# Performance work log

Hardware: AMD Instinct MI355X
Metric: run time of the kernel (lower is better)

Reference implementation:

```python
import jax, jax.numpy as jnp
import numpy as np

D_MODEL, HEADS, D_FF = 768, 12, 3072
D_K = D_MODEL // HEADS
EPS = 1e-6


def _norm(x, alpha, bias):
    # NormalizationLayer: scalar alpha/bias, torch.std is unbiased (ddof=1)
    mean = jnp.mean(x, axis=-1, keepdims=True)
    std = jnp.std(x, axis=-1, ddof=1, keepdims=True)
    return alpha * (x - mean) / (std + EPS) + bias


def setup_inputs() -> dict:
    key = jax.random.key(0)
    ks = jax.random.split(key, 16)
    B, S = 2, 4096
    x = jax.random.normal(ks[0], (B, S, D_MODEL), dtype=jnp.float32)
    mask = jax.random.randint(ks[1], (B, 1, 1, S), 0, 2, dtype=jnp.int32)
    w = lambda k, o, i: (jax.random.normal(k, (o, i), dtype=jnp.float32) * 0.02)
    return {
        "x": x, "mask": mask,
        "wq": w(ks[2], D_MODEL, D_MODEL), "bq": jnp.zeros((D_MODEL,), jnp.float32),
        "wk": w(ks[3], D_MODEL, D_MODEL), "bk": jnp.zeros((D_MODEL,), jnp.float32),
        "wv": w(ks[4], D_MODEL, D_MODEL), "bv": jnp.zeros((D_MODEL,), jnp.float32),
        "wo": w(ks[5], D_MODEL, D_MODEL), "bo": jnp.zeros((D_MODEL,), jnp.float32),
        "w1": w(ks[6], D_FF, D_MODEL), "b1": jnp.zeros((D_FF,), jnp.float32),
        "w2": w(ks[7], D_MODEL, D_FF), "b2": jnp.zeros((D_MODEL,), jnp.float32),
        "alpha1": jnp.ones((1,), jnp.float32), "beta1": jnp.ones((1,), jnp.float32),
        "alpha2": jnp.ones((1,), jnp.float32), "beta2": jnp.ones((1,), jnp.float32),
    }


def reference(x, mask, wq, bq, wk, bk, wv, bv, wo, bo, w1, b1, w2, b2,
              alpha1, beta1, alpha2, beta2):
    B, S, _ = x.shape

    # --- residual connection 0: pre-norm + self-attention ---
    h = _norm(x, alpha1, beta1)
    q = (h @ wq.T + bq).reshape(B, S, HEADS, D_K).transpose(0, 2, 1, 3)  # [B,H,S,dk]
    k = (h @ wk.T + bk).reshape(B, S, HEADS, D_K).transpose(0, 2, 1, 3)
    v = (h @ wv.T + bv).reshape(B, S, HEADS, D_K).transpose(0, 2, 1, 3)
    scores = jnp.einsum('bhqd,bhkd->bhqk', q, k) / jnp.sqrt(jnp.float32(D_K))
    scores = jnp.where(mask == 0, jnp.float32(-1e9), scores)
    attn = jax.nn.softmax(scores, axis=-1)
    ctx = jnp.einsum('bhqk,bhkd->bhqd', attn, v)
    ctx = ctx.transpose(0, 2, 1, 3).reshape(B, S, D_MODEL)
    x = x + (ctx @ wo.T + bo)

    # --- residual connection 1: pre-norm + FFN ---
    h = _norm(x, alpha2, beta2)
    ff = jax.nn.relu(h @ w1.T + b1) @ w2.T + b2
    return x + ff
```

## Files before the change

kernel.cpp:

```cpp
#include <hip/hip_runtime.h>
#include <hip/hip_bf16.h>
#include <math.h>


typedef __hip_bfloat16 bf16;
typedef short short8 __attribute__((ext_vector_type(8)));
typedef short short4v __attribute__((ext_vector_type(4)));
typedef float f32x4 __attribute__((ext_vector_type(4)));

#define MFMA(A, B, C) __builtin_amdgcn_mfma_f32_16x16x32_bf16(A, B, C, 0, 0, 0)

__device__ __forceinline__ void gl_lds16(const void* g, void* l) {
  __builtin_amdgcn_global_load_lds(
      (__attribute__((address_space(1))) void*)g,
      (__attribute__((address_space(3))) void*)l, 16, 0, 0);
}

__device__ __forceinline__ short f2b(float f) {
  bf16 h = __float2bfloat16(f);
  return *reinterpret_cast<short*>(&h);
}

__global__ __launch_bounds__(256)
void prep_all(const float* __restrict__ wq, const float* __restrict__ wk,
              const float* __restrict__ wv, const float* __restrict__ wo,
              const float* __restrict__ w1, const float* __restrict__ w2,
              const float* __restrict__ bq, const float* __restrict__ bk,
              const float* __restrict__ bv, const int* __restrict__ mask,
              bf16* __restrict__ wqkvb, bf16* __restrict__ wob,
              bf16* __restrict__ w1b, bf16* __restrict__ w2b,
              float* __restrict__ bqkv,
              int* __restrict__ pos_g, int* __restrict__ nch_g,
              float* __restrict__ biasc,
              bf16* __restrict__ kc, bf16* __restrict__ vtc)
{
  const int t = threadIdx.x;
  if (blockIdx.x < 2) {
    const int b = blockIdx.x;
    const int* mb = mask + b * 4096;
    __shared__ int lsum[256];
    int loc = 0;
    int mv[16];
#pragma unroll
    for (int j = 0; j < 16; j++) { mv[j] = mb[t * 16 + j] ? 1 : 0; loc += mv[j]; }
    lsum[t] = loc;
    __syncthreads();
    for (int off = 1; off < 256; off <<= 1) {
      int v = (t >= off) ? lsum[t - off] : 0;
      __syncthreads();
      lsum[t] += v;
      __syncthreads();
    }
    const int nvalid = lsum[255];
    int base = lsum[t] - loc;
#pragma unroll
    for (int j = 0; j < 16; j++) {
      pos_g[b * 4096 + t * 16 + j] = mv[j] ? base : -1;
      if (mv[j]) base++;
    }
    const int npad = (nvalid + 63) & ~63;
    if (t == 0) nch_g[b] = npad >> 6;
    for (int i = t; i < 4096; i += 256)
      biasc[b * 4096 + i] = (i < nvalid) ? 0.f : -1e9f;
    const int npv = npad - nvalid;
    if (npv > 0) {
      const int krows = 12 * npv;
      const short8 z = {};
      for (int task = t; task < krows * 8; task += 256) {
        const int rr = task >> 3, cc = task & 7;
        const int hh = rr / npv, r = nvalid + rr % npv;
        *(short8*)&kc[(((long)(b * 12 + hh) * 4096) + r) * 64 + cc * 8] = z;
      }
      const int vrows = 12 * 64;
      for (int task = t; task < vrows * npv; task += 256) {
        const int row = task / npv, j = nvalid + task % npv;
        const int hh = row >> 6, d = row & 63;
        vtc[((long)((b * 12 + hh) * 64 + d)) * 4096 + j] = __float2bfloat16(0.f);
      }
    }
    return;
  }
  const int i = (blockIdx.x - 2) * 256 + t;
  const int W = 147456;
  const int F = 589824;
  const float* src; bf16* dst; int off;
  if (i < W)          { src = wq; dst = wqkvb;           off = i; }
  else if (i < 2*W)   { src = wk; dst = wqkvb + 589824;  off = i - W; }
  else if (i < 3*W)   { src = wv; dst = wqkvb + 1179648; off = i - 2*W; }
  else if (i < 4*W)   { src = wo; dst = wob;             off = i - 3*W; }
  else if (i < 4*W+F) { src = w1; dst = w1b;             off = i - 4*W; }
  else                { src = w2; dst = w2b;             off = i - 4*W - F; }
  float4 v = ((const float4*)src)[off];
  short4v o;
  o.x = f2b(v.x); o.y = f2b(v.y); o.z = f2b(v.z); o.w = f2b(v.w);
  ((short4v*)dst)[off] = o;
  if (i < 2304)
    bqkv[i] = (i < 768) ? bq[i] : (i < 1536 ? bk[i - 768] : bv[i - 1536]);
}

template<typename INT>
__global__ __launch_bounds__(256)
void ln_kernel(const INT* __restrict__ x, bf16* __restrict__ out,
               const float* __restrict__ alpha, const float* __restrict__ beta)
{
  const int row = blockIdx.x;
  const long base = (long)row * 768;
  const int t = threadIdx.x;
  float v[3]; float s = 0.f, ss = 0.f;
#pragma unroll
  for (int i = 0; i < 3; i++) {
    v[i] = (float)x[base + t + i * 256];
    s += v[i]; ss += v[i] * v[i];
  }
#pragma unroll
  for (int off = 32; off > 0; off >>= 1) {
    s  += __shfl_down(s, off);
    ss += __shfl_down(ss, off);
  }
  __shared__ float red[8];
  __shared__ float stats[2];
  const int w = t >> 6;
  if ((t & 63) == 0) { red[w] = s; red[4 + w] = ss; }
  __syncthreads();
  if (t == 0) {
    float S  = red[0] + red[1] + red[2] + red[3];
    float SS = red[4] + red[5] + red[6] + red[7];
    float mean = S * (1.f / 768.f);
    float var = fmaxf((SS - 768.f * mean * mean) * (1.f / 767.f), 0.f);
    stats[0] = mean;
    stats[1] = 1.f / (sqrtf(var) + 1e-6f);
  }
  __syncthreads();
  const float mean = stats[0], rinv = stats[1];
  const float a = alpha[0], b = beta[0];
#pragma unroll
  for (int i = 0; i < 3; i++)
    out[base + t + i * 256] = __float2bfloat16(a * (v[i] - mean) * rinv + b);
}

template<int MODE, int TM, typename RT, typename OUTT>
__global__ __launch_bounds__(256)
void gemm_bt(const bf16* __restrict__ A, const bf16* __restrict__ W,
             const float* __restrict__ bias, const RT* __restrict__ R,
             OUTT* __restrict__ Cout, int M, int N, int K)
{
  constexpr int MI = TM / 32;
  __shared__ __align__(16) bf16 sA[TM * 32];
  __shared__ __align__(16) bf16 sB[128 * 32];
  const int t = threadIdx.x;
  const int w = t >> 6, lane = t & 63;
  const int lr = lane & 15, quad = lane >> 4;
  const int tm = blockIdx.x * TM, tn = blockIdx.y * 128;
  const int wm = (w >> 1) * (MI * 16), wn = (w & 1) * 64;

  const int srow = w * 16 + (lane >> 2);
  const int scol = (lane & 3) * 8;
  const bf16* Ap = A + (long)(tm + srow) * K + scol;
  const bf16* Wp = W + (long)(tn + srow) * K + scol;
  bf16* sAp = &sA[srow * 32 + scol];
  bf16* sBp = &sB[srow * 32 + scol];
  const long half = (long)64 * K;

  f32x4 acc[MI][4] = {};

  for (int kb = 0; kb < K; kb += 32) {
    gl_lds16(Ap + kb, sAp);
    if (TM == 128) gl_lds16(Ap + kb + half, sAp + 64 * 32);
    gl_lds16(Wp + kb, sBp);
    gl_lds16(Wp + kb + half, sBp + 64 * 32);
    __syncthreads();
    short8 af[MI], bfr[4];
#pragma unroll
    for (int i = 0; i < MI; i++)
      af[i] = *(const short8*)&sA[(wm + i * 16 + lr) * 32 + quad * 8];
#pragma unroll
    for (int j = 0; j < 4; j++)
      bfr[j] = *(const short8*)&sB[(wn + j * 16 + lr) * 32 + quad * 8];
#pragma unroll
    for (int i = 0; i < MI; i++)
#pragma unroll
      for (int j = 0; j < 4; j++)
        acc[i][j] = MFMA(af[i], bfr[j], acc[i][j]);
    __syncthreads();
  }

#pragma unroll
  for (int i = 0; i < MI; i++) {
#pragma unroll
    for (int j = 0; j < 4; j++) {
      const int col = tn + wn + j * 16 + lr;
      const float bv = bias[col];
#pragma unroll
      for (int r = 0; r < 4; r++) {
        const int m = tm + wm + i * 16 + quad * 4 + r;
        float vv = acc[i][j][r] + bv;
        if (MODE == 1) vv = fmaxf(vv, 0.f);
        if (MODE == 4) vv += (float)R[(long)m * N + col];
        Cout[(long)m * N + col] = (OUTT)vv;
      }
    }
  }
}

__global__ __launch_bounds__(256)
void gemm_qkv(const bf16* __restrict__ A, const bf16* __restrict__ W,
              const float* __restrict__ bias, const int* __restrict__ pos_g,
              bf16* __restrict__ Qo, bf16* __restrict__ Kc, bf16* __restrict__ Vtc)
{
  const int K = 768;
  __shared__ __align__(16) bf16 sA[128 * 32];
  __shared__ __align__(16) bf16 sB[128 * 32];
  const int t = threadIdx.x;
  const int w = t >> 6, lane = t & 63;
  const int lr = lane & 15, quad = lane >> 4;
  const int tm = blockIdx.x * 128, tn = blockIdx.y * 128;
  const int wm = (w >> 1) * 64, wn = (w & 1) * 64;

  const int srow = w * 16 + (lane >> 2);
  const int scol = (lane & 3) * 8;
  const bf16* Ap = A + (long)(tm + srow) * K + scol;
  const bf16* Wp = W + (long)(tn + srow) * K + scol;
  bf16* sAp = &sA[srow * 32 + scol];
  bf16* sBp = &sB[srow * 32 + scol];
  const long half = (long)64 * K;

  f32x4 acc[4][4] = {};

  for (int kb = 0; kb < K; kb += 32) {
    gl_lds16(Ap + kb, sAp);
    gl_lds16(Ap + kb + half, sAp + 64 * 32);
    gl_lds16(Wp + kb, sBp);
    gl_lds16(Wp + kb + half, sBp + 64 * 32);
    __syncthreads();
    short8 af[4], bfr[4];
#pragma unroll
    for (int i = 0; i < 4; i++)
      af[i] = *(const short8*)&sA[(wm + i * 16 + lr) * 32 + quad * 8];
#pragma unroll
    for (int j = 0; j < 4; j++)
      bfr[j] = *(const short8*)&sB[(wn + j * 16 + lr) * 32 + quad * 8];
#pragma unroll
    for (int i = 0; i < 4; i++)
#pragma unroll
      for (int j = 0; j < 4; j++)
        acc[i][j] = MFMA(af[i], bfr[j], acc[i][j]);
    __syncthreads();
  }

  const int region = (tn >= 1536) ? 2 : (tn >= 768 ? 1 : 0);
#pragma unroll
  for (int i = 0; i < 4; i++) {
#pragma unroll
    for (int j = 0; j < 4; j++) {
      const int col = tn + wn + j * 16 + lr;
      const int c768 = col - region * 768;
      const int hh = c768 >> 6, d = c768 & 63;
      const float bv = bias[col];
#pragma unroll
      for (int r = 0; r < 4; r++) {
        const int m = tm + wm + i * 16 + quad * 4 + r;
        const int bb = m >> 12, sdx = m & 4095;
        float vv = acc[i][j][r] + bv;
        if (region == 0) {
          vv *= 0.125f;
          Qo[((long)(bb * 12 + hh) * 4096 + sdx) * 64 + d] = __float2bfloat16(vv);
        } else {
          const int p_ = pos_g[bb * 4096 + sdx];
          if (p_ >= 0) {
            if (region == 1)
              Kc[((long)(bb * 12 + hh) * 4096 + p_) * 64 + d] = __float2bfloat16(vv);
            else
              Vtc[((long)(bb * 12 + hh) * 64 + d) * 4096 + p_] = __float2bfloat16(vv);
          }
        }
      }
    }
  }
}

__global__ __launch_bounds__(256)
void attn_kernel(const bf16* __restrict__ Q, const bf16* __restrict__ Kg,
                 const bf16* __restrict__ Vt, const float* __restrict__ biasc,
                 const int* __restrict__ nch_g, bf16* __restrict__ ctx)
{
  __shared__ __align__(16) bf16 sK[64 * 72];
  __shared__ __align__(16) bf16 sV[64 * 72];
  __shared__ __align__(16) bf16 sP[4][32 * 72];

  const int t = threadIdx.x, w = t >> 6, lane = t & 63;
  const int lr = lane & 15, quad = lane >> 4;
  const int bh = blockIdx.y, b = bh / 12, hh = bh % 12;
  const int qb = blockIdx.x * 128 + w * 32;
  const long bh_s = (long)bh * 4096;
  const float* bg = biasc + b * 4096;
  const int nch = nch_g[b];

  short8 qf[2][2];
#pragma unroll
  for (int qt = 0; qt < 2; qt++) {
    const bf16* qp = Q + (bh_s + qb + qt * 16 + lr) * 64 + quad * 8;
    qf[qt][0] = *(const short8*)qp;
    qf[qt][1] = *(const short8*)(qp + 32);
  }

  float l_part[2][4] = {};
  f32x4 O[2][4] = {};

  const int srow = t >> 3;
  const int scol = (t & 7) * 8;
  const bf16* kp0 = Kg + (bh_s + srow) * 64 + scol;
  const bf16* kp1 = Kg + (bh_s + srow + 32) * 64 + scol;
  const bf16* vp0 = Vt + ((long)bh * 64 + srow) * 4096 + scol;
  const bf16* vp1 = Vt + ((long)bh * 64 + srow + 32) * 4096 + scol;

  for (int ci = 0; ci < nch; ci++) {
    const int kc = ci * 64;
    short8 k0 = *(const short8*)(kp0 + (long)kc * 64);
    short8 k1 = *(const short8*)(kp1 + (long)kc * 64);
    short8 v0 = *(const short8*)(vp0 + kc);
    short8 v1 = *(const short8*)(vp1 + kc);
    float bb[4];
#pragma unroll
    for (int kt = 0; kt < 4; kt++) bb[kt] = bg[kc + kt * 16 + lr];
    __syncthreads();
    *(short8*)&sK[srow * 72 + scol]        = k0;
    *(short8*)&sK[(srow + 32) * 72 + scol] = k1;
    *(short8*)&sV[srow * 72 + scol]        = v0;
    *(short8*)&sV[(srow + 32) * 72 + scol] = v1;
    __syncthreads();

    f32x4 s[2][4] = {};
#pragma unroll
    for (int kt = 0; kt < 4; kt++) {
      short8 kfa = *(const short8*)&sK[(kt * 16 + lr) * 72 + quad * 8];
      short8 kfb = *(const short8*)&sK[(kt * 16 + lr) * 72 + 32 + quad * 8];
      s[0][kt] = MFMA(qf[0][0], kfa, s[0][kt]);
      s[0][kt] = MFMA(qf[0][1], kfb, s[0][kt]);
      s[1][kt] = MFMA(qf[1][0], kfa, s[1][kt]);
      s[1][kt] = MFMA(qf[1][1], kfb, s[1][kt]);
    }

#pragma unroll
    for (int kt = 0; kt < 4; kt++) {
#pragma unroll
      for (int qt = 0; qt < 2; qt++) {
#pragma unroll
        for (int r = 0; r < 4; r++) {
          const float p = __expf(s[qt][kt][r] + bb[kt]);
          l_part[qt][r] += p;
          sP[w][(qt * 16 + quad * 4 + r) * 72 + kt * 16 + lr] = __float2bfloat16(p);
        }
      }
    }

    short8 pf[2][2];
#pragma unroll
    for (int qt = 0; qt < 2; qt++) {
      pf[qt][0] = *(const short8*)&sP[w][(qt * 16 + lr) * 72 + quad * 8];
      pf[qt][1] = *(const short8*)&sP[w][(qt * 16 + lr) * 72 + 32 + quad * 8];
    }
#pragma unroll
    for (int j = 0; j < 4; j++) {
      short8 vfa = *(const short8*)&sV[(j * 16 + lr) * 72 + quad * 8];
      short8 vfb = *(const short8*)&sV[(j * 16 + lr) * 72 + 32 + quad * 8];
      O[0][j] = MFMA(pf[0][0], vfa, O[0][j]);
      O[0][j] = MFMA(pf[0][1], vfb, O[0][j]);
      O[1][j] = MFMA(pf[1][0], vfa, O[1][j]);
      O[1][j] = MFMA(pf[1][1], vfb, O[1][j]);
    }
  }

#pragma unroll
  for (int qt = 0; qt < 2; qt++) {
#pragma unroll
    for (int r = 0; r < 4; r++) {
      float l = l_part[qt][r];
#pragma unroll
      for (int off = 1; off < 16; off <<= 1) l += __shfl_xor(l, off, 16);
      const float il = (l > 0.f) ? 1.f / l : 0.f;
      const int q = qb + qt * 16 + quad * 4 + r;
      bf16* cp = ctx + ((long)(b * 4096 + q)) * 768 + hh * 64 + lr;
#pragma unroll
      for (int j = 0; j < 4; j++)
        cp[j * 16] = __float2bfloat16(O[qt][j][r] * il);
    }
  }
}

extern "C" void kernel_launch(void* const* d_in, const int* in_sizes, int n_in,
                              void* d_out, int out_size, void* d_ws, size_t ws_size,
                              hipStream_t stream)
{
  (void)in_sizes; (void)n_in; (void)out_size; (void)ws_size;
  const float* x    = (const float*)d_in[0];
  const int*   mask = (const int*)  d_in[1];
  const float* wq = (const float*)d_in[2];  const float* bq = (const float*)d_in[3];
  const float* wk = (const float*)d_in[4];  const float* bk = (const float*)d_in[5];
  const float* wv = (const float*)d_in[6];  const float* bv = (const float*)d_in[7];
  const float* wo = (const float*)d_in[8];  const float* bo = (const float*)d_in[9];
  const float* w1 = (const float*)d_in[10]; const float* b1 = (const float*)d_in[11];
  const float* w2 = (const float*)d_in[12]; const float* b2 = (const float*)d_in[13];
  const float* alpha1 = (const float*)d_in[14]; const float* beta1 = (const float*)d_in[15];
  const float* alpha2 = (const float*)d_in[16]; const float* beta2 = (const float*)d_in[17];
  float* out = (float*)d_out;

  const long WSZ = (long)768 * 768 * 2;
  const long W1SZ = (long)3072 * 768 * 2;
  const long SZB = (long)8192 * 768 * 2;
  char* ws = (char*)d_ws;
  bf16* wqkvb = (bf16*)(ws);
  bf16* wob = (bf16*)(ws + 3 * WSZ);
  bf16* w1b = (bf16*)(ws + 4 * WSZ);
  bf16* w2b = (bf16*)(ws + 4 * WSZ + W1SZ);
  char* aux = ws + 4 * WSZ + 2 * W1SZ;
  float* bqkv   = (float*)(aux);
  int*   pos_g  = (int*)(aux + 16384);
  float* biasc  = (float*)(aux + 49152);
  int*   nch_g  = (int*)(aux + 81920);
  const long BASE = 16l << 20;
  bf16* h   = (bf16*)(ws + BASE);
  bf16* qws = (bf16*)(ws + BASE + 1 * SZB);
  bf16* kcw = (bf16*)(ws + BASE + 2 * SZB);
  bf16* vtc = (bf16*)(ws + BASE + 3 * SZB);
  bf16* ctx = (bf16*)(ws + BASE + 4 * SZB);
  bf16* x1  = (bf16*)(ws + BASE + 5 * SZB);
  bf16* ff  = qws;

  dim3 blk(256);

  hipLaunchKernelGGL(prep_all, dim3(6914), blk, 0, stream,
                     wq, wk, wv, wo, w1, w2, bq, bk, bv, mask,
                     wqkvb, wob, w1b, w2b, bqkv, pos_g, nch_g, biasc, kcw, vtc);

  hipLaunchKernelGGL((ln_kernel<float>), dim3(8192), blk, 0, stream, x, h, alpha1, beta1);
  hipLaunchKernelGGL(gemm_qkv, dim3(64, 18), blk, 0, stream, h, wqkvb, bqkv, pos_g, qws, kcw, vtc);
  hipLaunchKernelGGL(attn_kernel, dim3(32, 24), blk, 0, stream, qws, kcw, vtc, biasc, nch_g, ctx);
  hipLaunchKernelGGL((gemm_bt<4, 64, float, bf16>), dim3(128, 6), blk, 0, stream, ctx, wob, bo, x, x1, 8192, 768, 768);
  hipLaunchKernelGGL((ln_kernel<bf16>), dim3(8192), blk, 0, stream, x1, h, alpha2, beta2);
  hipLaunchKernelGGL((gemm_bt<1, 128, float, bf16>), dim3(64, 24), blk, 0, stream, h, w1b, b1, (const float*)nullptr, ff, 8192, 3072, 768);
  hipLaunchKernelGGL((gemm_bt<4, 64, bf16, float>), dim3(128, 6), blk, 0, stream, ff, w2b, b2, x1, out, 8192, 768, 3072);
}
```

Before: 425.9 us.

## Double-buffer attention K/V via async LDS loads with swizzled layout and exp2

```diff
diff --git a/kernel.cpp b/kernel.cpp
--- a/kernel.cpp
+++ b/kernel.cpp
@@ -9,6 +9,12 @@
 typedef float f32x4 __attribute__((ext_vector_type(4)));
 
 #define MFMA(A, B, C) __builtin_amdgcn_mfma_f32_16x16x32_bf16(A, B, C, 0, 0, 0)
+
+#if __has_builtin(__builtin_amdgcn_exp2f)
+#define EXP2(x) __builtin_amdgcn_exp2f(x)
+#else
+#define EXP2(x) exp2f(x)
+#endif
 
 __device__ __forceinline__ void gl_lds16(const void* g, void* l) {
   __builtin_amdgcn_global_load_lds(
@@ -262,7 +268,7 @@
         const int bb = m >> 12, sdx = m & 4095;
         float vv = acc[i][j][r] + bv;
         if (region == 0) {
-          vv *= 0.125f;
+          vv *= 0.18033688011112042f;
           Qo[((long)(bb * 12 + hh) * 4096 + sdx) * 64 + d] = __float2bfloat16(vv);
         } else {
           const int p_ = pos_g[bb * 4096 + sdx];
@@ -283,9 +289,9 @@
                  const bf16* __restrict__ Vt, const float* __restrict__ biasc,
                  const int* __restrict__ nch_g, bf16* __restrict__ ctx)
 {
-  __shared__ __align__(16) bf16 sK[64 * 72];
-  __shared__ __align__(16) bf16 sV[64 * 72];
-  __shared__ __align__(16) bf16 sP[4][32 * 72];
+  __shared__ __align__(16) bf16 sK[2][64 * 64];
+  __shared__ __align__(16) bf16 sV[2][64 * 64];
+  __shared__ __align__(16) bf16 sP[4][32 * 64];
 
   const int t = threadIdx.x, w = t >> 6, lane = t & 63;
   const int lr = lane & 15, quad = lane >> 4;
@@ -294,6 +300,7 @@
   const long bh_s = (long)bh * 4096;
   const float* bg = biasc + b * 4096;
   const int nch = nch_g[b];
+  bf16* sPw = sP[w];
 
   short8 qf[2][2];
 #pragma unroll
@@ -303,72 +310,94 @@
     qf[qt][1] = *(const short8*)(qp + 32);
   }
 
+  const int rA = w * 16 + (lane >> 3), rB = rA + 8;
+  const int c8 = lane & 7;
+  const int sigA = ((rA & 15) << 2) + (rA >> 4);
+  const int sigB = ((rB & 15) << 2) + (rB >> 4);
+  const bf16* kA = Kg + (bh_s + sigA) * 64 + ((c8 ^ (rA & 7)) << 3);
+  const bf16* kB = Kg + (bh_s + sigB) * 64 + ((c8 ^ (rB & 7)) << 3);
+  const bf16* vA = Vt + ((long)bh * 64 + rA) * 4096 + ((c8 ^ (rA & 7)) << 3);
+  const bf16* vB = Vt + ((long)bh * 64 + rB) * 4096 + ((c8 ^ (rB & 7)) << 3);
+  const int ldsA = (w * 16) * 64 + lane * 8;
+  const int ldsB = ldsA + 8 * 64;
+
+  const int cA = (quad * 8) ^ ((lr & 7) << 3);
+
   float l_part[2][4] = {};
   f32x4 O[2][4] = {};
 
-  const int srow = t >> 3;
-  const int scol = (t & 7) * 8;
-  const bf16* kp0 = Kg + (bh_s + srow) * 64 + scol;
-  const bf16* kp1 = Kg + (bh_s + srow + 32) * 64 + scol;
-  const bf16* vp0 = Vt + ((long)bh * 64 + srow) * 4096 + scol;
-  const bf16* vp1 = Vt + ((long)bh * 64 + srow + 32) * 4096 + scol;
-
-  for (int ci = 0; ci < nch; ci++) {
-    const int kc = ci * 64;
-    short8 k0 = *(const short8*)(kp0 + (long)kc * 64);
-    short8 k1 = *(const short8*)(kp1 + (long)kc * 64);
-    short8 v0 = *(const short8*)(vp0 + kc);
-    short8 v1 = *(const short8*)(vp1 + kc);
-    float bb[4];
-#pragma unroll
-    for (int kt = 0; kt < 4; kt++) bb[kt] = bg[kc + kt * 16 + lr];
-    __syncthreads();
-    *(short8*)&sK[srow * 72 + scol]        = k0;
-    *(short8*)&sK[(srow + 32) * 72 + scol] = k1;
-    *(short8*)&sV[srow * 72 + scol]        = v0;
-    *(short8*)&sV[(srow + 32) * 72 + scol] = v1;
-    __syncthreads();
-
+  auto stage = [&](int kc, int buf) {
+    gl_lds16(kA + (long)kc * 64, &sK[buf][ldsA]);
+    gl_lds16(kB + (long)kc * 64, &sK[buf][ldsB]);
+    gl_lds16(vA + kc, &sV[buf][ldsA]);
+    gl_lds16(vB + kc, &sV[buf][ldsB]);
+  };
+
+  auto compute = [&](int kc, int buf, bool dobias) {
+    const bf16* Kb = sK[buf];
+    const bf16* Vb = sV[buf];
     f32x4 s[2][4] = {};
 #pragma unroll
     for (int kt = 0; kt < 4; kt++) {
-      short8 kfa = *(const short8*)&sK[(kt * 16 + lr) * 72 + quad * 8];
-      short8 kfb = *(const short8*)&sK[(kt * 16 + lr) * 72 + 32 + quad * 8];
+      const int rowb = (kt * 16 + lr) * 64;
+      short8 kfa = *(const short8*)&Kb[rowb + cA];
+      short8 kfb = *(const short8*)&Kb[rowb + (cA ^ 32)];
       s[0][kt] = MFMA(qf[0][0], kfa, s[0][kt]);
       s[0][kt] = MFMA(qf[0][1], kfb, s[0][kt]);
       s[1][kt] = MFMA(qf[1][0], kfa, s[1][kt]);
       s[1][kt] = MFMA(qf[1][1], kfb, s[1][kt]);
     }
-
-#pragma unroll
-    for (int kt = 0; kt < 4; kt++) {
-#pragma unroll
-      for (int qt = 0; qt < 2; qt++) {
-#pragma unroll
-        for (int r = 0; r < 4; r++) {
-          const float p = __expf(s[qt][kt][r] + bb[kt]);
-          l_part[qt][r] += p;
-          sP[w][(qt * 16 + quad * 4 + r) * 72 + kt * 16 + lr] = __float2bfloat16(p);
+    float bb0 = 0.f, bb1 = 0.f, bb2 = 0.f, bb3 = 0.f;
+    if (dobias) {
+      const float4 b4 = *(const float4*)&bg[kc + lr * 4];
+      bb0 = b4.x; bb1 = b4.y; bb2 = b4.z; bb3 = b4.w;
+    }
+#pragma unroll
+    for (int qt = 0; qt < 2; qt++) {
+#pragma unroll
+      for (int r = 0; r < 4; r++) {
+        float p0, p1, p2, p3;
+        if (dobias) {
+          p0 = EXP2(s[qt][0][r] + bb0); p1 = EXP2(s[qt][1][r] + bb1);
+          p2 = EXP2(s[qt][2][r] + bb2); p3 = EXP2(s[qt][3][r] + bb3);
+        } else {
+          p0 = EXP2(s[qt][0][r]); p1 = EXP2(s[qt][1][r]);
+          p2 = EXP2(s[qt][2][r]); p3 = EXP2(s[qt][3][r]);
         }
+        l_part[qt][r] += (p0 + p1) + (p2 + p3);
+        const int q = qt * 16 + quad * 4 + r;
+        short4v pw;
+        pw.x = f2b(p0); pw.y = f2b(p1); pw.z = f2b(p2); pw.w = f2b(p3);
+        *(short4v*)&sPw[q * 64 + ((lr * 4) ^ ((q & 7) << 3))] = pw;
       }
     }
-
     short8 pf[2][2];
 #pragma unroll
     for (int qt = 0; qt < 2; qt++) {
-      pf[qt][0] = *(const short8*)&sP[w][(qt * 16 + lr) * 72 + quad * 8];
-      pf[qt][1] = *(const short8*)&sP[w][(qt * 16 + lr) * 72 + 32 + quad * 8];
+      const int rowb = (qt * 16 + lr) * 64;
+      pf[qt][0] = *(const short8*)&sPw[rowb + cA];
+      pf[qt][1] = *(const short8*)&sPw[rowb + (cA ^ 32)];
     }
 #pragma unroll
     for (int j = 0; j < 4; j++) {
-      short8 vfa = *(const short8*)&sV[(j * 16 + lr) * 72 + quad * 8];
-      short8 vfb = *(const short8*)&sV[(j * 16 + lr) * 72 + 32 + quad * 8];
+      const int rowb = (j * 16 + lr) * 64;
+      short8 vfa = *(const short8*)&Vb[rowb + cA];
+      short8 vfb = *(const short8*)&Vb[rowb + (cA ^ 32)];
       O[0][j] = MFMA(pf[0][0], vfa, O[0][j]);
       O[0][j] = MFMA(pf[0][1], vfb, O[0][j]);
       O[1][j] = MFMA(pf[1][0], vfa, O[1][j]);
       O[1][j] = MFMA(pf[1][1], vfb, O[1][j]);
     }
-  }
+  };
+
+  stage(0, 0);
+  for (int ci = 0; ci < nch - 1; ci++) {
+    __syncthreads();
+    stage((ci + 1) * 64, (ci + 1) & 1);
+    compute(ci * 64, ci & 1, false);
+  }
+  __syncthreads();
+  if (nch > 0) compute((nch - 1) * 64, (nch - 1) & 1, true);
 
 #pragma unroll
   for (int qt = 0; qt < 2; qt++) {
```

After: 407.3 us. -4.4%, faster.
